# Kernel optimization log

Measured on AMD Instinct MI355X. Metric: run time of the kernel, lower is better.

Reference implementation:

```python
import jax, jax.numpy as jnp
import numpy as np

N_NODES = 100000
IN_CH = 2048
OUT_CH = 128
ITERATIONS = 4
NNZ_FEAT = 2000000
NNZ_ADJ = 1600000


def setup_inputs() -> dict:
    key = jax.random.key(0)
    ks = jax.random.split(key, 8)
    feat_rows = jax.random.randint(ks[0], (NNZ_FEAT,), 0, N_NODES, dtype=jnp.int64 if jax.config.jax_enable_x64 else jnp.int32)
    feat_cols = jax.random.randint(ks[1], (NNZ_FEAT,), 0, IN_CH, dtype=feat_rows.dtype)
    feat_values = jax.random.uniform(ks[2], (NNZ_FEAT,), dtype=jnp.float32)
    adj_rows = jax.random.randint(ks[3], (NNZ_ADJ,), 0, N_NODES, dtype=feat_rows.dtype)
    adj_cols = jax.random.randint(ks[4], (NNZ_ADJ,), 0, N_NODES, dtype=feat_rows.dtype)
    # normalized adjacency values ~ 1/degree scale
    adj_values = jax.random.uniform(ks[5], (NNZ_ADJ,), dtype=jnp.float32) * (1.0 / 16.0)
    # xavier_uniform for weight [in, out] and bias [1, out]
    wb = float(np.sqrt(6.0 / (IN_CH + OUT_CH)))
    weight = jax.random.uniform(ks[6], (IN_CH, OUT_CH), minval=-wb, maxval=wb, dtype=jnp.float32)
    bb = float(np.sqrt(6.0 / (1 + OUT_CH)))
    bias = jax.random.uniform(ks[7], (1, OUT_CH), minval=-bb, maxval=bb, dtype=jnp.float32)
    return {
        "feat_rows": feat_rows, "feat_cols": feat_cols, "feat_values": feat_values,
        "adj_rows": adj_rows, "adj_cols": adj_cols, "adj_values": adj_values,
        "weight": weight, "bias": bias,
    }


def _spmm(rows, cols, values, dense, n_out_rows):
    # COO sparse [n_out_rows, *] @ dense [*, d] -> [n_out_rows, d]
    contrib = values[:, None] * dense[cols]  # [nnz, d]
    return jax.ops.segment_sum(contrib, rows, num_segments=n_out_rows)


def reference(feat_rows, feat_cols, feat_values, adj_rows, adj_cols, adj_values, weight, bias):
    # base = spmm(sparse_features, W) + b ; dropout is identity in eval mode
    h = _spmm(feat_rows, feat_cols, feat_values, weight, N_NODES)  # [N, out]
    h = jax.nn.relu(h + bias)
    for _ in range(ITERATIONS - 1):
        h = _spmm(adj_rows, adj_cols, adj_values, h, N_NODES)
    return h
```

## Files before the change

### kernel.cpp

```cpp
#include <hip/hip_runtime.h>
#include <hip/hip_fp16.h>

#define N_NODES 100000
#define IN_CH 2048
#define OUT_CH 128
#define NNZ_FEAT 2000000
#define NNZ_ADJ 1600000
#define NNZ_TOT (NNZ_FEAT + NNZ_ADJ)
#define BROWS 512
#define NBUCK 391
#define NROWP (NBUCK * BROWS)
#define BCAP 12288
#define KB_BLOCK 512
#define KB_ITEMS 8
#define KB_CHUNK (KB_BLOCK * KB_ITEMS)
#define KB_GRID ((NNZ_TOT + KB_CHUNK - 1) / KB_CHUNK)

#define PK_COL_BITS 17
#define PK_COL_MASK ((1 << PK_COL_BITS) - 1)


__global__ void k_init(int* __restrict__ gcur) {
    int t = threadIdx.x;
    if (t < NBUCK) gcur[t] = t * BCAP;
}


__global__ __launch_bounds__(KB_BLOCK) void kB(const int* __restrict__ frows,
                                               const int* __restrict__ fcols,
                                               const float* __restrict__ fvals,
                                               const int* __restrict__ arows,
                                               const int* __restrict__ acols,
                                               const float* __restrict__ avals,
                                               int* __restrict__ gcur,
                                               int* __restrict__ tmp_pk,
                                               float* __restrict__ tmp_vl) {
    __shared__ int hist[NBUCK];
    __shared__ int lcnt[NBUCK];
    __shared__ int gb[NBUCK];
    __shared__ int bstart[NBUCK];
    __shared__ int sc[512];
    __shared__ int s_pk[KB_CHUNK];
    __shared__ float s_vl[KB_CHUNK];
    __shared__ unsigned short s_bid[KB_CHUNK];

    int tid = threadIdx.x;
    if (tid < NBUCK) { hist[tid] = 0; lcnt[tid] = 0; }
    __syncthreads();

    long base = (long)blockIdx.x * KB_CHUNK;
    int rr[KB_ITEMS];
    for (int j = 0; j < KB_ITEMS; ++j) {
        long i = base + j * KB_BLOCK + tid;
        int r = -1;
        if (i < NNZ_TOT) {
            r = (i < NNZ_FEAT) ? frows[i] : (N_NODES + arows[i - NNZ_FEAT]);
            atomicAdd(&hist[r >> 9], 1);
        }
        rr[j] = r;
    }
    __syncthreads();

    sc[tid] = (tid < NBUCK) ? hist[tid] : 0;
    __syncthreads();
    for (int o = 1; o < 512; o <<= 1) {
        int x = (tid >= o) ? sc[tid - o] : 0;
        __syncthreads();
        sc[tid] += x;
        __syncthreads();
    }
    if (tid < NBUCK) {
        int h = hist[tid];
        bstart[tid] = sc[tid] - h;
        gb[tid] = h ? atomicAdd(&gcur[tid], h) : 0;
    }
    __syncthreads();
    int tot = sc[NBUCK - 1];

    for (int j = 0; j < KB_ITEMS; ++j) {
        int r = rr[j];
        if (r >= 0) {
            long i = base + j * KB_BLOCK + tid;
            int c; float v;
            if (i < NNZ_FEAT) { c = fcols[i]; v = fvals[i]; }
            else              { c = acols[i - NNZ_FEAT]; v = avals[i - NNZ_FEAT]; }
            int b = r >> 9;
            int slot = bstart[b] + atomicAdd(&lcnt[b], 1);
            s_pk[slot] = ((r & 511) << PK_COL_BITS) | c;
            s_vl[slot] = v;
            s_bid[slot] = (unsigned short)b;
        }
    }
    __syncthreads();

    for (int s = tid; s < tot; s += KB_BLOCK) {
        int b = s_bid[s];
        int dest = gb[b] + (s - bstart[b]);
        tmp_pk[dest] = s_pk[s];
        tmp_vl[dest] = s_vl[s];
    }
}


__global__ void k_scand(const int* __restrict__ gcur, int* __restrict__ dstart) {
    __shared__ int s[512];
    int t = threadIdx.x;
    int cnt = (t < NBUCK) ? (gcur[t] - t * BCAP) : 0;
    s[t] = cnt;
    __syncthreads();
    for (int o = 1; o < 512; o <<= 1) {
        int x = (t >= o) ? s[t - o] : 0;
        __syncthreads();
        s[t] += x;
        __syncthreads();
    }
    if (t < NBUCK) dstart[t] = s[t] - cnt;
}


__global__ __launch_bounds__(512) void kC(const int* __restrict__ gcur,
                                          const int* __restrict__ dstart,
                                          const int* __restrict__ tmp_pk,
                                          const float* __restrict__ tmp_vl,
                                          int2* __restrict__ pairs,
                                          int* __restrict__ S) {
    __shared__ int rcnt[BROWS];
    __shared__ int sc2[BROWS];
    __shared__ int rcur[BROWS];
    int tid = threadIdx.x;
    int b = blockIdx.x, rbase = b << 9;
    rcnt[tid] = 0;
    __syncthreads();
    int e0 = b * BCAP;
    int e1 = e0 + (gcur[b] - b * BCAP);
    int dbase = dstart[b];
    for (int i = e0 + tid; i < e1; i += 512)
        atomicAdd(&rcnt[tmp_pk[i] >> PK_COL_BITS], 1);
    __syncthreads();
    sc2[tid] = rcnt[tid];
    __syncthreads();
    for (int o = 1; o < 512; o <<= 1) {
        int x = (tid >= o) ? sc2[tid - o] : 0;
        __syncthreads();
        sc2[tid] += x;
        __syncthreads();
    }
    int ex0 = dbase + sc2[tid] - rcnt[tid];
    S[rbase + tid] = ex0;
    rcur[tid] = ex0;
    __syncthreads();
    for (int i = e0 + tid; i < e1; i += 512) {
        int pk = tmp_pk[i];
        float v = tmp_vl[i];
        int p = atomicAdd(&rcur[pk >> PK_COL_BITS], 1);
        pairs[p] = make_int2(pk & PK_COL_MASK, __float_as_int(v));
    }
}


__global__ __launch_bounds__(256) void k_wconv(const float* __restrict__ W,
                                               __half2* __restrict__ Wh) {
    int i = blockIdx.x * 256 + threadIdx.x;
    if (i < IN_CH * OUT_CH / 2) {
        float2 f = ((const float2*)W)[i];
        Wh[i] = __floats2half2_rn(f.x, f.y);
    }
}


#define SPMM_GROUP(OFS)                                                        \
    _Pragma("unroll")                                                          \
    for (int j = 0; j < 8; ++j) {                                              \
        int c = __builtin_amdgcn_readlane(pp.x, (OFS) + j);                    \
        float v = __int_as_float(__builtin_amdgcn_readlane(pp.y, (OFS) + j));  \
        float2 f = __half22float2(HSRC_AT(c));                                 \
        if (j & 1) { a1.x = fmaf(v, f.x, a1.x); a1.y = fmaf(v, f.y, a1.y); }   \
        else       { a0.x = fmaf(v, f.x, a0.x); a0.y = fmaf(v, f.y, a0.y); }   \
    }

#define SPMM_BODY(ACC_INIT)                                                    \
    int row = blockIdx.x * 4 + (threadIdx.x >> 6);                             \
    int lane = threadIdx.x & 63;                                               \
    int k0 = __builtin_amdgcn_readfirstlane(SROW0);                            \
    int k1 = __builtin_amdgcn_readfirstlane(SROW1);                            \
    float2 a0 = ACC_INIT;                                                      \
    float2 a1 = make_float2(0.0f, 0.0f);                                       \
    for (int base = k0; base < k1; base += 64) {                               \
        int idx = base + lane;                                                 \
        int2 pp = (idx < k1) ? pairs[idx] : make_int2(0, 0);                   \
        int n = k1 - base; if (n > 64) n = 64;                                 \
        int full = n & ~7;                                                     \
        for (int jj = 0; jj < full; jj += 8) { SPMM_GROUP(jj) }                \
        if (full < n) { SPMM_GROUP(full) }                                     \
    }

__global__ __launch_bounds__(256) void spmm_w(const int* __restrict__ S,
                                              const int2* __restrict__ pairs,
                                              const __half2* __restrict__ Wh,
                                              const float* __restrict__ bias,
                                              __half2* __restrict__ out16) {
#define SROW0 S[row]
#define SROW1 S[row + 1]
#define HSRC_AT(c) Wh[(size_t)(c) * (OUT_CH / 2) + lane]
    SPMM_BODY(((const float2*)bias)[lane])
#undef HSRC_AT
#undef SROW0
#undef SROW1
    float rx = fmaxf(a0.x + a1.x, 0.0f);
    float ry = fmaxf(a0.y + a1.y, 0.0f);
    out16[(size_t)row * (OUT_CH / 2) + lane] = __floats2half2_rn(rx, ry);
}

__global__ __launch_bounds__(256) void spmm_adj_hh(const int* __restrict__ S,
                                                   const int2* __restrict__ pairs,
                                                   const __half2* __restrict__ hin,
                                                   __half2* __restrict__ hout) {
#define SROW0 S[N_NODES + row]
#define SROW1 S[N_NODES + row + 1]
#define HSRC_AT(c) hin[(size_t)(c) * (OUT_CH / 2) + lane]
    SPMM_BODY(make_float2(0.0f, 0.0f))
#undef HSRC_AT
#undef SROW0
#undef SROW1
    hout[(size_t)row * (OUT_CH / 2) + lane] = __floats2half2_rn(a0.x + a1.x, a0.y + a1.y);
}

__global__ __launch_bounds__(256) void spmm_adj_hf(const int* __restrict__ S,
                                                   const int2* __restrict__ pairs,
                                                   const __half2* __restrict__ hin,
                                                   float* __restrict__ out) {
#define SROW0 S[N_NODES + row]
#define SROW1 S[N_NODES + row + 1]
#define HSRC_AT(c) hin[(size_t)(c) * (OUT_CH / 2) + lane]
    SPMM_BODY(make_float2(0.0f, 0.0f))
#undef HSRC_AT
#undef SROW0
#undef SROW1
    float2 acc;
    acc.x = a0.x + a1.x;
    acc.y = a0.y + a1.y;
    ((float2*)(out + (size_t)row * OUT_CH))[lane] = acc;
}


extern "C" void kernel_launch(void* const* d_in, const int* in_sizes, int n_in,
                              void* d_out, int out_size, void* d_ws, size_t ws_size,
                              hipStream_t stream) {
    const int*   frows = (const int*)d_in[0];
    const int*   fcols = (const int*)d_in[1];
    const float* fvals = (const float*)d_in[2];
    const int*   arows = (const int*)d_in[3];
    const int*   acols = (const int*)d_in[4];
    const float* avals = (const float*)d_in[5];
    const float* W     = (const float*)d_in[6];
    const float* bias  = (const float*)d_in[7];
    float* out = (float*)d_out;

    char* ws = (char*)d_ws;
    size_t off = 0;
    auto alloc = [&](size_t bytes) {
        size_t o = off;
        off = (off + bytes + 255) & ~(size_t)255;
        return o;
    };
    int*  S      = (int*) (ws + alloc((size_t)NROWP * 4));
    int*  gcur   = (int*) (ws + alloc(512 * 4));
    int*  dstart = (int*) (ws + alloc(512 * 4));
    int2* pairs  = (int2*)(ws + alloc((size_t)NNZ_TOT * 8));
    __half2* Wh  = (__half2*)(ws + alloc((size_t)IN_CH * OUT_CH * 2));
    char* hraw   = ws + alloc(2 * (size_t)N_NODES * OUT_CH * 2);
    __half2* hA  = (__half2*)hraw;
    __half2* hB  = (__half2*)(hraw + (size_t)N_NODES * OUT_CH * 2);
    int*   tmp_pk = (int*)hraw;
    float* tmp_vl = (float*)(hraw + (((size_t)NBUCK * BCAP * 4 + 255) & ~(size_t)255));
    (void)ws_size; (void)off; (void)in_sizes; (void)n_in; (void)out_size;

    k_init<<<1, 512, 0, stream>>>(gcur);
    k_wconv<<<(IN_CH * OUT_CH / 2 + 255) / 256, 256, 0, stream>>>(W, Wh);
    kB<<<KB_GRID, KB_BLOCK, 0, stream>>>(frows, fcols, fvals, arows, acols, avals,
                                         gcur, tmp_pk, tmp_vl);
    k_scand<<<1, 512, 0, stream>>>(gcur, dstart);
    kC<<<NBUCK, 512, 0, stream>>>(gcur, dstart, tmp_pk, tmp_vl, pairs, S);

    spmm_w<<<N_NODES / 4, 256, 0, stream>>>(S, pairs, Wh, bias, hA);

    spmm_adj_hh<<<N_NODES / 4, 256, 0, stream>>>(S, pairs, hA, hB);
    spmm_adj_hh<<<N_NODES / 4, 256, 0, stream>>>(S, pairs, hB, hA);
    spmm_adj_hf<<<N_NODES / 4, 256, 0, stream>>>(S, pairs, hA, out);
}
```

Before: 294.9 us.

## Pack bucket temp as int2, cache bucket in registers, grid-stride SpMM kernels

The bucketing temp buffer now stores key and value together as one int2 instead of two separate arrays. kC loads its whole bucket once into registers (up to 24 items per thread), so the second pass over the bucket does not re-read global memory. The four SpMM kernels switch from one block per 4 rows to a fixed grid of 4096 blocks that stride over the rows. The register cache raises VGPR pressure in kC, and it silently drops items if a bucket holds more than 12288 entries, which is the same limit as BCAP.

```diff
diff --git a/kernel.cpp b/kernel.cpp
--- a/kernel.cpp
+++ b/kernel.cpp
@@ -11,10 +11,12 @@
 #define NBUCK 391
 #define NROWP (NBUCK * BROWS)
 #define BCAP 12288
+#define KC_MAX 24
 #define KB_BLOCK 512
 #define KB_ITEMS 8
 #define KB_CHUNK (KB_BLOCK * KB_ITEMS)
 #define KB_GRID ((NNZ_TOT + KB_CHUNK - 1) / KB_CHUNK)
+#define SPMM_GRID 4096
 
 #define PK_COL_BITS 17
 #define PK_COL_MASK ((1 << PK_COL_BITS) - 1)
@@ -33,8 +35,7 @@
                                                const int* __restrict__ acols,
                                                const float* __restrict__ avals,
                                                int* __restrict__ gcur,
-                                               int* __restrict__ tmp_pk,
-                                               float* __restrict__ tmp_vl) {
+                                               int2* __restrict__ tmp) {
     __shared__ int hist[NBUCK];
     __shared__ int lcnt[NBUCK];
     __shared__ int gb[NBUCK];
@@ -96,8 +97,7 @@
     for (int s = tid; s < tot; s += KB_BLOCK) {
         int b = s_bid[s];
         int dest = gb[b] + (s - bstart[b]);
-        tmp_pk[dest] = s_pk[s];
-        tmp_vl[dest] = s_vl[s];
+        tmp[dest] = make_int2(s_pk[s], __float_as_int(s_vl[s]));
     }
 }
 
@@ -120,8 +120,7 @@
 
 __global__ __launch_bounds__(512) void kC(const int* __restrict__ gcur,
                                           const int* __restrict__ dstart,
-                                          const int* __restrict__ tmp_pk,
-                                          const float* __restrict__ tmp_vl,
+                                          const int2* __restrict__ tmp,
                                           int2* __restrict__ pairs,
                                           int* __restrict__ S) {
     __shared__ int rcnt[BROWS];
@@ -132,10 +131,19 @@
     rcnt[tid] = 0;
     __syncthreads();
     int e0 = b * BCAP;
-    int e1 = e0 + (gcur[b] - b * BCAP);
+    int cnt = gcur[b] - e0;
     int dbase = dstart[b];
-    for (int i = e0 + tid; i < e1; i += 512)
-        atomicAdd(&rcnt[tmp_pk[i] >> PK_COL_BITS], 1);
+
+    int2 it[KC_MAX];
+#pragma unroll
+    for (int i = 0; i < KC_MAX; ++i) {
+        int idx = i * 512 + tid;
+        if (idx < cnt) it[i] = tmp[e0 + idx];
+    }
+#pragma unroll
+    for (int i = 0; i < KC_MAX; ++i) {
+        if (i * 512 + tid < cnt) atomicAdd(&rcnt[it[i].x >> PK_COL_BITS], 1);
+    }
     __syncthreads();
     sc2[tid] = rcnt[tid];
     __syncthreads();
@@ -149,11 +157,12 @@
     S[rbase + tid] = ex0;
     rcur[tid] = ex0;
     __syncthreads();
-    for (int i = e0 + tid; i < e1; i += 512) {
-        int pk = tmp_pk[i];
-        float v = tmp_vl[i];
-        int p = atomicAdd(&rcur[pk >> PK_COL_BITS], 1);
-        pairs[p] = make_int2(pk & PK_COL_MASK, __float_as_int(v));
+#pragma unroll
+    for (int i = 0; i < KC_MAX; ++i) {
+        if (i * 512 + tid < cnt) {
+            int p = atomicAdd(&rcur[it[i].x >> PK_COL_BITS], 1);
+            pairs[p] = make_int2(it[i].x & PK_COL_MASK, it[i].y);
+        }
     }
 }
 
@@ -178,11 +187,10 @@
         else       { a0.x = fmaf(v, f.x, a0.x); a0.y = fmaf(v, f.y, a0.y); }   \
     }
 
-#define SPMM_BODY(ACC_INIT)                                                    \
-    int row = blockIdx.x * 4 + (threadIdx.x >> 6);                             \
-    int lane = threadIdx.x & 63;                                               \
-    int k0 = __builtin_amdgcn_readfirstlane(SROW0);                            \
-    int k1 = __builtin_amdgcn_readfirstlane(SROW1);                            \
+#define SPMM_ROW(SOFS, ACC_INIT)                                               \
+    int row = rg * 4 + wid;                                                    \
+    int k0 = __builtin_amdgcn_readfirstlane(S[(SOFS) + row]);                  \
+    int k1 = __builtin_amdgcn_readfirstlane(S[(SOFS) + row + 1]);              \
     float2 a0 = ACC_INIT;                                                      \
     float2 a1 = make_float2(0.0f, 0.0f);                                       \
     for (int base = k0; base < k1; base += 64) {                               \
@@ -199,47 +207,45 @@
                                               const __half2* __restrict__ Wh,
                                               const float* __restrict__ bias,
                                               __half2* __restrict__ out16) {
-#define SROW0 S[row]
-#define SROW1 S[row + 1]
+    int wid = threadIdx.x >> 6, lane = threadIdx.x & 63;
+    float2 binit = ((const float2*)bias)[lane];
+    for (int rg = blockIdx.x; rg < N_NODES / 4; rg += SPMM_GRID) {
 #define HSRC_AT(c) Wh[(size_t)(c) * (OUT_CH / 2) + lane]
-    SPMM_BODY(((const float2*)bias)[lane])
+        SPMM_ROW(0, binit)
 #undef HSRC_AT
-#undef SROW0
-#undef SROW1
-    float rx = fmaxf(a0.x + a1.x, 0.0f);
-    float ry = fmaxf(a0.y + a1.y, 0.0f);
-    out16[(size_t)row * (OUT_CH / 2) + lane] = __floats2half2_rn(rx, ry);
+        float rx = fmaxf(a0.x + a1.x, 0.0f);
+        float ry = fmaxf(a0.y + a1.y, 0.0f);
+        out16[(size_t)row * (OUT_CH / 2) + lane] = __floats2half2_rn(rx, ry);
+    }
 }
 
 __global__ __launch_bounds__(256) void spmm_adj_hh(const int* __restrict__ S,
                                                    const int2* __restrict__ pairs,
                                                    const __half2* __restrict__ hin,
                                                    __half2* __restrict__ hout) {
-#define SROW0 S[N_NODES + row]
-#define SROW1 S[N_NODES + row + 1]
+    int wid = threadIdx.x >> 6, lane = threadIdx.x & 63;
+    for (int rg = blockIdx.x; rg < N_NODES / 4; rg += SPMM_GRID) {
 #define HSRC_AT(c) hin[(size_t)(c) * (OUT_CH / 2) + lane]
-    SPMM_BODY(make_float2(0.0f, 0.0f))
+        SPMM_ROW(N_NODES, make_float2(0.0f, 0.0f))
 #undef HSRC_AT
-#undef SROW0
-#undef SROW1
-    hout[(size_t)row * (OUT_CH / 2) + lane] = __floats2half2_rn(a0.x + a1.x, a0.y + a1.y);
+        hout[(size_t)row * (OUT_CH / 2) + lane] = __floats2half2_rn(a0.x + a1.x, a0.y + a1.y);
+    }
 }
 
 __global__ __launch_bounds__(256) void spmm_adj_hf(const int* __restrict__ S,
                                                    const int2* __restrict__ pairs,
                                                    const __half2* __restrict__ hin,
                                                    float* __restrict__ out) {
-#define SROW0 S[N_NODES + row]
-#define SROW1 S[N_NODES + row + 1]
+    int wid = threadIdx.x >> 6, lane = threadIdx.x & 63;
+    for (int rg = blockIdx.x; rg < N_NODES / 4; rg += SPMM_GRID) {
 #define HSRC_AT(c) hin[(size_t)(c) * (OUT_CH / 2) + lane]
-    SPMM_BODY(make_float2(0.0f, 0.0f))
+        SPMM_ROW(N_NODES, make_float2(0.0f, 0.0f))
 #undef HSRC_AT
-#undef SROW0
-#undef SROW1
-    float2 acc;
-    acc.x = a0.x + a1.x;
-    acc.y = a0.y + a1.y;
-    ((float2*)(out + (size_t)row * OUT_CH))[lane] = acc;
+        float2 acc;
+        acc.x = a0.x + a1.x;
+        acc.y = a0.y + a1.y;
+        ((float2*)(out + (size_t)row * OUT_CH))[lane] = acc;
+    }
 }
 
 
@@ -271,20 +277,19 @@
     char* hraw   = ws + alloc(2 * (size_t)N_NODES * OUT_CH * 2);
     __half2* hA  = (__half2*)hraw;
     __half2* hB  = (__half2*)(hraw + (size_t)N_NODES * OUT_CH * 2);
-    int*   tmp_pk = (int*)hraw;
-    float* tmp_vl = (float*)(hraw + (((size_t)NBUCK * BCAP * 4 + 255) & ~(size_t)255));
+    int2* tmp = (int2*)hraw;
     (void)ws_size; (void)off; (void)in_sizes; (void)n_in; (void)out_size;
 
     k_init<<<1, 512, 0, stream>>>(gcur);
     k_wconv<<<(IN_CH * OUT_CH / 2 + 255) / 256, 256, 0, stream>>>(W, Wh);
     kB<<<KB_GRID, KB_BLOCK, 0, stream>>>(frows, fcols, fvals, arows, acols, avals,
-                                         gcur, tmp_pk, tmp_vl);
+                                         gcur, tmp);
     k_scand<<<1, 512, 0, stream>>>(gcur, dstart);
-    kC<<<NBUCK, 512, 0, stream>>>(gcur, dstart, tmp_pk, tmp_vl, pairs, S);
-
-    spmm_w<<<N_NODES / 4, 256, 0, stream>>>(S, pairs, Wh, bias, hA);
-
-    spmm_adj_hh<<<N_NODES / 4, 256, 0, stream>>>(S, pairs, hA, hB);
-    spmm_adj_hh<<<N_NODES / 4, 256, 0, stream>>>(S, pairs, hB, hA);
-    spmm_adj_hf<<<N_NODES / 4, 256, 0, stream>>>(S, pairs, hA, out);
-}
+    kC<<<NBUCK, 512, 0, stream>>>(gcur, dstart, tmp, pairs, S);
+
+    spmm_w<<<SPMM_GRID, 256, 0, stream>>>(S, pairs, Wh, bias, hA);
+
+    spmm_adj_hh<<<SPMM_GRID, 256, 0, stream>>>(S, pairs, hA, hB);
+    spmm_adj_hh<<<SPMM_GRID, 256, 0, stream>>>(S, pairs, hB, hA);
+    spmm_adj_hf<<<SPMM_GRID, 256, 0, stream>>>(S, pairs, hA, out);
+}
```

New measurement: 289.8 us. No clear change (-1.7%).
